# Kernel optimization log

Hardware: AMD Instinct MI355X
Metric: run time of the kernel (lower is better)

The kernel has to match this reference:

```python
import jax, jax.numpy as jnp
import numpy as np

NUM_HEADS = 16
NEG_INF = -1000000.0  # matches torch masked_fill value


def setup_inputs() -> dict:
    key = jax.random.key(0)
    k1, k2, k3, k4, k5, k6 = jax.random.split(key, 6)
    N, S, E = 2, 2048, 1024
    x_encoder = jax.random.normal(k1, (N, S, E), dtype=jnp.float32)
    x_decoder = jax.random.normal(k2, (N, S, E), dtype=jnp.float32)
    mask = jax.random.randint(k3, (S, S), 0, 2, dtype=jnp.int32)
    W_qk = jax.random.normal(k4, (2 * E, E), dtype=jnp.float32) * (1.0 / np.sqrt(E))
    W_v = jax.random.normal(k5, (E, E), dtype=jnp.float32) * (1.0 / np.sqrt(E))
    W_o = jax.random.normal(k6, (E, E), dtype=jnp.float32) * (1.0 / np.sqrt(E))
    return {"x_encoder": x_encoder, "x_decoder": x_decoder, "mask": mask,
            "W_qk": W_qk, "W_v": W_v, "W_o": W_o}


def reference(x_encoder, x_decoder, mask, W_qk, W_v, W_o):
    N, S, E = x_encoder.shape
    H = NUM_HEADS
    hd = E // H
    # projections (no bias)
    qk = x_encoder @ W_qk.T            # (N, S, 2E)
    v = x_decoder @ W_v.T              # (N, S, E)
    qk = qk.reshape(N, S, H, 2 * hd).transpose(0, 2, 1, 3)  # (N, H, S, 2hd)
    v = v.reshape(N, S, H, hd).transpose(0, 2, 1, 3)         # (N, H, S, hd)
    q, k = qk[..., :hd], qk[..., hd:]
    # scaled dot-product attention with mask fill
    logits = jnp.einsum('bhqd,bhkd->bhqk', q, k) / jnp.sqrt(jnp.float32(hd))
    m = mask[None, None, :, :]  # expand_mask: 2D -> (1,1,S,S)
    logits = jnp.where(m == 0, jnp.float32(NEG_INF), logits)
    attn = jax.nn.softmax(logits, axis=-1)
    vals = jnp.einsum('bhqk,bhkd->bhqd', attn, v)            # (N, H, S, hd)
    vals = vals.transpose(0, 2, 1, 3).reshape(N, S, E)
    return vals @ W_o.T
```

## Files before the change

### kernel.cpp

```cpp
#include <hip/hip_runtime.h>

typedef __attribute__((ext_vector_type(8))) short short8;
typedef __attribute__((ext_vector_type(4))) float f32x4;
typedef __attribute__((ext_vector_type(4))) unsigned short u16x4;
typedef __attribute__((ext_vector_type(4))) unsigned int u32x4;

#define MFMA16(A,B,C) __builtin_amdgcn_mfma_f32_16x16x32_bf16(A,B,C,0,0,0)

__device__ __forceinline__ unsigned short f2bf(float f) {
  unsigned int u = __builtin_bit_cast(unsigned int, f);
  unsigned int r = (u + 0x7fffu + ((u >> 16) & 1u)) >> 16;
  return (unsigned short)r;
}

__device__ __forceinline__ unsigned int cvt_pk_bf16(float lo, float hi) {
  unsigned int r;
  asm("v_cvt_pk_bf16_f32 %0, %1, %2" : "=v"(r) : "v"(lo), "v"(hi));
  return r;
}

__device__ __forceinline__ f32x4 zero4() {
  f32x4 z; z.x = 0.f; z.y = 0.f; z.z = 0.f; z.w = 0.f; return z;
}

__device__ __forceinline__ void gl_lds16(const void* g, void* l) {
  __builtin_amdgcn_global_load_lds((const __attribute__((address_space(1))) void*)g,
                                   (__attribute__((address_space(3))) void*)l, 16, 0, 0);
}

__global__ __launch_bounds__(256) void cvt_all(const float* __restrict__ xe,
                                               const float* __restrict__ xd,
                                               const float* __restrict__ wqk,
                                               const float* __restrict__ wv,
                                               const float* __restrict__ wo,
                                               unsigned short* __restrict__ ws) {
  long i = (long)blockIdx.x * 256 + threadIdx.x;
  const float* src; unsigned short* dst; long o;
  if (i < 1048576)      { src = xe;  dst = ws;            o = i; }
  else if (i < 2097152) { src = xd;  dst = ws + 4194304;  o = i - 1048576; }
  else if (i < 2621440) { src = wqk; dst = ws + 8388608;  o = i - 2097152; }
  else if (i < 2883584) { src = wv;  dst = ws + 10485760; o = i - 2621440; }
  else                  { src = wo;  dst = ws + 11534336; o = i - 2883584; }
  float4 f = ((const float4*)src)[o];
  u16x4 r; r.x = f2bf(f.x); r.y = f2bf(f.y); r.z = f2bf(f.z); r.w = f2bf(f.w);
  ((u16x4*)dst)[o] = r;
}

__global__ __launch_bounds__(256) void mask_pack(const int* __restrict__ mask,
                                                 unsigned int* __restrict__ mbits) {
  int idx = blockIdx.x * 256 + threadIdx.x;
  int row = idx >> 6, wi = idx & 63;
  const int* p = mask + (long)row * 2048 + wi * 32;
  unsigned int bits = 0;
  #pragma unroll
  for (int j = 0; j < 32; j++) bits |= (p[j] != 0 ? 1u : 0u) << j;
  mbits[idx] = bits;
}

template <int MODE>
__global__ __launch_bounds__(256) void gemm_bt(const unsigned short* __restrict__ A,
                                               const unsigned short* __restrict__ B,
                                               void* __restrict__ Cv,
                                               int M, int N, int K) {
  __shared__ __align__(16) unsigned short As[128 * 64];
  __shared__ __align__(16) unsigned short Bs[128 * 64];
  const int tid = threadIdx.x;
  const int w = tid >> 6, l = tid & 63;
  const int wr = w >> 1, wc = w & 1;
  const long row0 = (long)blockIdx.y * 128;
  const long col0 = (long)blockIdx.x * 128;
  const int lr = l >> 3;
  const int lc = (l & 7) * 8;

  f32x4 acc[4][4];
  #pragma unroll
  for (int m = 0; m < 4; m++)
    #pragma unroll
    for (int n = 0; n < 4; n++) acc[m][n] = zero4();

  for (int k0 = 0; k0 < K; k0 += 64) {
    #pragma unroll
    for (int j = 0; j < 4; j++) {
      int slot = j * 4 + w;
      int row = slot * 8 + lr;
      gl_lds16(A + (row0 + row) * K + k0 + lc, &As[slot * 512]);
      gl_lds16(B + (col0 + row) * K + k0 + lc, &Bs[slot * 512]);
    }
    __syncthreads();
    #pragma unroll
    for (int kk = 0; kk < 2; kk++) {
      short8 a[4], b[4];
      #pragma unroll
      for (int m = 0; m < 4; m++)
        a[m] = *(const short8*)&As[(wr * 64 + m * 16 + (l & 15)) * 64 + kk * 32 + (l >> 4) * 8];
      #pragma unroll
      for (int n = 0; n < 4; n++)
        b[n] = *(const short8*)&Bs[(wc * 64 + n * 16 + (l & 15)) * 64 + kk * 32 + (l >> 4) * 8];
      #pragma unroll
      for (int m = 0; m < 4; m++)
        #pragma unroll
        for (int n = 0; n < 4; n++)
          acc[m][n] = MFMA16(a[m], b[n], acc[m][n]);
    }
    __syncthreads();
  }

  #pragma unroll
  for (int m = 0; m < 4; m++) {
    long rowb = row0 + wr * 64 + m * 16 + ((l >> 4) * 4);
    #pragma unroll
    for (int n = 0; n < 4; n++) {
      long colb = col0 + wc * 64 + n * 16 + (l & 15);
      if (MODE == 0) {
        unsigned short* C = (unsigned short*)Cv;
        #pragma unroll
        for (int r = 0; r < 4; r++) C[(rowb + r) * N + colb] = f2bf(acc[m][n][r]);
      } else if (MODE == 1) {
        unsigned short* C = (unsigned short*)Cv;
        long bb = rowb >> 11, s0 = rowb & 2047;
        u16x4 pk;
        pk.x = f2bf(acc[m][n][0]); pk.y = f2bf(acc[m][n][1]);
        pk.z = f2bf(acc[m][n][2]); pk.w = f2bf(acc[m][n][3]);
        *(u16x4*)&C[(bb * 1024 + colb) * 2048 + s0] = pk;
      } else {
        float* C = (float*)Cv;
        #pragma unroll
        for (int r = 0; r < 4; r++) C[(rowb + r) * N + colb] = acc[m][n][r];
      }
    }
  }
}

__global__ __launch_bounds__(256, 4) void attn(const unsigned short* __restrict__ qk,
                                               const unsigned short* __restrict__ vT,
                                               const unsigned int* __restrict__ mbits,
                                               unsigned short* __restrict__ vals) {
  __shared__ __align__(16) unsigned short Ks[2][64 * 64];
  __shared__ __align__(16) unsigned short Vs[2][64 * 64];
  const int tid = threadIdx.x;
  const int w = tid >> 6, l = tid & 63;
  const int b = blockIdx.z, h = blockIdx.y;
  const int q0 = blockIdx.x * 64;
  const int c = l & 15, g = l >> 4;
  const int lr = l >> 3, pg = l & 7;

  const int qrow = q0 + w * 16 + c;
  const unsigned short* qptr = qk + (long)(b * 2048 + qrow) * 2048 + h * 128;
  short8 bq0 = *(const short8*)&qptr[g * 8];
  short8 bq1 = *(const short8*)&qptr[32 + g * 8];

  const float SC = 0.125f * 1.4426950408889634f;
  const int sw0 = ((g)     ^ (c & 7)) * 8;
  const int sw1 = ((g + 4) ^ (c & 7)) * 8;
  const int sA = c + (((2 * g)     & 3) << 4);
  const int sB = c + (((2 * g + 1) & 3) << 4);
  const int gh = g >> 1;

  const unsigned int* mrowp = mbits + (long)qrow * 64;

  const unsigned short* kbase = qk + (long)b * 2048 * 2048 + h * 128 + 64;
  const unsigned short* vbase = vT + (long)((b * 16 + h) * 64) * 2048;
  const int srow = w * 8 + lr;
  const int sgg = pg ^ (lr & 7);

  float l_run = 0.f;
  f32x4 o[4];
  #pragma unroll
  for (int d = 0; d < 4; d++) o[d] = zero4();

  {
    #pragma unroll
    for (int j = 0; j < 2; j++) {
      int row = srow + j * 32;
      gl_lds16(kbase + (long)row * 2048 + sgg * 8, &Ks[0][(w + j * 4) * 512]);
      gl_lds16(vbase + (long)row * 2048 + sgg * 8, &Vs[0][(w + j * 4) * 512]);
    }
  }
  __syncthreads();

  for (int kv0 = 0; kv0 < 2048; kv0 += 64) {
    const int cur = (kv0 >> 6) & 1;

    if (kv0 + 64 < 2048) {
      #pragma unroll
      for (int j = 0; j < 2; j++) {
        int row = srow + j * 32;
        gl_lds16(kbase + (long)(kv0 + 64 + row) * 2048 + sgg * 8, &Ks[cur ^ 1][(w + j * 4) * 512]);
        gl_lds16(vbase + (long)row * 2048 + kv0 + 64 + sgg * 8, &Vs[cur ^ 1][(w + j * 4) * 512]);
      }
    }

    unsigned long long mw = *(const unsigned long long*)&mrowp[kv0 >> 5];

    f32x4 sf[4];
    #pragma unroll
    for (int kvq = 0; kvq < 4; kvq++) {
      int R = kvq * 16 + c;
      short8 ak0 = *(const short8*)&Ks[cur][R * 64 + sw0];
      short8 ak1 = *(const short8*)&Ks[cur][R * 64 + sw1];
      f32x4 z = zero4();
      z = MFMA16(ak0, bq0, z);
      z = MFMA16(ak1, bq1, z);
      sf[kvq] = z;
    }

    mw >>= (g * 4);
    unsigned int mlo = (unsigned int)mw, mhi = (unsigned int)(mw >> 32);
    float pv[16];
    float lsum = 0.f;
    #pragma unroll
    for (int kvq = 0; kvq < 4; kvq++) {
      unsigned int msel = (kvq < 2) ? mlo : mhi;
      #pragma unroll
      for (int r = 0; r < 4; r++) {
        float e = __builtin_amdgcn_exp2f(sf[kvq][r] * SC);
        unsigned int bit = (msel >> (((kvq & 1) << 4) + r)) & 1u;
        float p = bit ? e : 0.0f;
        pv[kvq * 4 + r] = p;
        lsum += p;
      }
    }
    l_run += lsum;

    unsigned int pk0[2], pk1[2], pk2[2], pk3[2];
    pk0[0] = cvt_pk_bf16(pv[0],  pv[1]);  pk0[1] = cvt_pk_bf16(pv[2],  pv[3]);
    pk1[0] = cvt_pk_bf16(pv[4],  pv[5]);  pk1[1] = cvt_pk_bf16(pv[6],  pv[7]);
    pk2[0] = cvt_pk_bf16(pv[8],  pv[9]);  pk2[1] = cvt_pk_bf16(pv[10], pv[11]);
    pk3[0] = cvt_pk_bf16(pv[12], pv[13]); pk3[1] = cvt_pk_bf16(pv[14], pv[15]);

    u32x4 a0, a1;
    {
      int t0, t1;
      t0 = __shfl((int)pk0[0], sA); t1 = __shfl((int)pk1[0], sA);
      a0.x = gh ? (unsigned)t1 : (unsigned)t0;
      t0 = __shfl((int)pk0[1], sA); t1 = __shfl((int)pk1[1], sA);
      a0.y = gh ? (unsigned)t1 : (unsigned)t0;
      t0 = __shfl((int)pk0[0], sB); t1 = __shfl((int)pk1[0], sB);
      a0.z = gh ? (unsigned)t1 : (unsigned)t0;
      t0 = __shfl((int)pk0[1], sB); t1 = __shfl((int)pk1[1], sB);
      a0.w = gh ? (unsigned)t1 : (unsigned)t0;
      t0 = __shfl((int)pk2[0], sA); t1 = __shfl((int)pk3[0], sA);
      a1.x = gh ? (unsigned)t1 : (unsigned)t0;
      t0 = __shfl((int)pk2[1], sA); t1 = __shfl((int)pk3[1], sA);
      a1.y = gh ? (unsigned)t1 : (unsigned)t0;
      t0 = __shfl((int)pk2[0], sB); t1 = __shfl((int)pk3[0], sB);
      a1.z = gh ? (unsigned)t1 : (unsigned)t0;
      t0 = __shfl((int)pk2[1], sB); t1 = __shfl((int)pk3[1], sB);
      a1.w = gh ? (unsigned)t1 : (unsigned)t0;
    }
    short8 pa0 = __builtin_bit_cast(short8, a0);
    short8 pa1 = __builtin_bit_cast(short8, a1);

    #pragma unroll
    for (int dt = 0; dt < 4; dt++) {
      int d = dt * 16 + c;
      short8 bv0 = *(const short8*)&Vs[cur][d * 64 + sw0];
      short8 bv1 = *(const short8*)&Vs[cur][d * 64 + sw1];
      o[dt] = MFMA16(pa0, bv0, o[dt]);
      o[dt] = MFMA16(pa1, bv1, o[dt]);
    }

    __syncthreads();
  }

  l_run += __shfl_xor(l_run, 16);
  l_run += __shfl_xor(l_run, 32);
  float linv = 1.0f / l_run;
  float l0 = __shfl(linv, g * 4 + 0);
  float l1 = __shfl(linv, g * 4 + 1);
  float l2 = __shfl(linv, g * 4 + 2);
  float l3 = __shfl(linv, g * 4 + 3);
  #pragma unroll
  for (int dt = 0; dt < 4; dt++) {
    long rowb = (long)b * 2048 + q0 + w * 16 + g * 4;
    int col = h * 64 + dt * 16 + c;
    vals[(rowb + 0) * 1024 + col] = f2bf(o[dt][0] * l0);
    vals[(rowb + 1) * 1024 + col] = f2bf(o[dt][1] * l1);
    vals[(rowb + 2) * 1024 + col] = f2bf(o[dt][2] * l2);
    vals[(rowb + 3) * 1024 + col] = f2bf(o[dt][3] * l3);
  }
}

extern "C" void kernel_launch(void* const* d_in, const int* in_sizes, int n_in,
                              void* d_out, int out_size, void* d_ws, size_t ws_size,
                              hipStream_t stream) {
  const float* xe  = (const float*)d_in[0];
  const float* xd  = (const float*)d_in[1];
  const int*   msk = (const int*)d_in[2];
  const float* wqk = (const float*)d_in[3];
  const float* wv  = (const float*)d_in[4];
  const float* wo  = (const float*)d_in[5];
  float* out = (float*)d_out;
  unsigned short* ws = (unsigned short*)d_ws;

  unsigned short* xe_bf  = ws;
  unsigned short* xd_bf  = ws + 4194304;
  unsigned short* wqk_bf = ws + 8388608;
  unsigned short* wv_bf  = ws + 10485760;
  unsigned short* wo_bf  = ws + 11534336;
  unsigned short* qkb    = ws + 12582912;
  unsigned short* vTb    = ws + 20971520;
  unsigned short* valb   = ws + 25165824;
  unsigned int*   mbits  = (unsigned int*)(ws + 29360128);

  cvt_all<<<12288, 256, 0, stream>>>(xe, xd, wqk, wv, wo, ws);
  mask_pack<<<512, 256, 0, stream>>>(msk, mbits);
  gemm_bt<0><<<dim3(16, 32), 256, 0, stream>>>(xe_bf, wqk_bf, qkb, 4096, 2048, 1024);
  gemm_bt<1><<<dim3(8, 32), 256, 0, stream>>>(xd_bf, wv_bf, vTb, 4096, 1024, 1024);
  attn<<<dim3(32, 16, 2), 256, 0, stream>>>(qkb, vTb, mbits, valb);
  gemm_bt<2><<<dim3(8, 32), 256, 0, stream>>>(valb, wo_bf, out, 4096, 1024, 1024);
}
```

Baseline: 167.3 us.

## Process two query tiles per wave and load V fragments directly from global

Each attention block now covers 128 query rows, with each wave handling two 16-row query tiles that share the same K tile in LDS. The V tile is no longer staged in shared memory. Each lane reads its V fragments straight from global memory into registers every iteration, which halves LDS usage and removes V LDS reads. The cost is more registers (occupancy hint lowered from 4 to 2), half as many blocks, and uncoalesced global V loads that are issued before the QK MFMAs and sit on the critical path.

```diff
diff --git a/kernel.cpp b/kernel.cpp
--- a/kernel.cpp
+++ b/kernel.cpp
@@ -131,23 +131,75 @@
   }
 }
 
-__global__ __launch_bounds__(256, 4) void attn(const unsigned short* __restrict__ qk,
+__device__ __forceinline__ void softmax_pack(const f32x4* sf, unsigned long long mw,
+                                             int g, int sA, int sB, int gh, float SC,
+                                             float& l_run, short8& pa0o, short8& pa1o) {
+  mw >>= (g * 4);
+  unsigned int mlo = (unsigned int)mw, mhi = (unsigned int)(mw >> 32);
+  float pv[16];
+  float lsum = 0.f;
+  #pragma unroll
+  for (int kvq = 0; kvq < 4; kvq++) {
+    unsigned int msel = (kvq < 2) ? mlo : mhi;
+    #pragma unroll
+    for (int r = 0; r < 4; r++) {
+      float e = __builtin_amdgcn_exp2f(sf[kvq][r] * SC);
+      unsigned int bit = (msel >> (((kvq & 1) << 4) + r)) & 1u;
+      float p = bit ? e : 0.0f;
+      pv[kvq * 4 + r] = p;
+      lsum += p;
+    }
+  }
+  l_run += lsum;
+
+  unsigned int pk0[2], pk1[2], pk2[2], pk3[2];
+  pk0[0] = cvt_pk_bf16(pv[0],  pv[1]);  pk0[1] = cvt_pk_bf16(pv[2],  pv[3]);
+  pk1[0] = cvt_pk_bf16(pv[4],  pv[5]);  pk1[1] = cvt_pk_bf16(pv[6],  pv[7]);
+  pk2[0] = cvt_pk_bf16(pv[8],  pv[9]);  pk2[1] = cvt_pk_bf16(pv[10], pv[11]);
+  pk3[0] = cvt_pk_bf16(pv[12], pv[13]); pk3[1] = cvt_pk_bf16(pv[14], pv[15]);
+
+  u32x4 a0, a1;
+  int t0, t1;
+  t0 = __shfl((int)pk0[0], sA); t1 = __shfl((int)pk1[0], sA);
+  a0.x = gh ? (unsigned)t1 : (unsigned)t0;
+  t0 = __shfl((int)pk0[1], sA); t1 = __shfl((int)pk1[1], sA);
+  a0.y = gh ? (unsigned)t1 : (unsigned)t0;
+  t0 = __shfl((int)pk0[0], sB); t1 = __shfl((int)pk1[0], sB);
+  a0.z = gh ? (unsigned)t1 : (unsigned)t0;
+  t0 = __shfl((int)pk0[1], sB); t1 = __shfl((int)pk1[1], sB);
+  a0.w = gh ? (unsigned)t1 : (unsigned)t0;
+  t0 = __shfl((int)pk2[0], sA); t1 = __shfl((int)pk3[0], sA);
+  a1.x = gh ? (unsigned)t1 : (unsigned)t0;
+  t0 = __shfl((int)pk2[1], sA); t1 = __shfl((int)pk3[1], sA);
+  a1.y = gh ? (unsigned)t1 : (unsigned)t0;
+  t0 = __shfl((int)pk2[0], sB); t1 = __shfl((int)pk3[0], sB);
+  a1.z = gh ? (unsigned)t1 : (unsigned)t0;
+  t0 = __shfl((int)pk2[1], sB); t1 = __shfl((int)pk3[1], sB);
+  a1.w = gh ? (unsigned)t1 : (unsigned)t0;
+  pa0o = __builtin_bit_cast(short8, a0);
+  pa1o = __builtin_bit_cast(short8, a1);
+}
+
+__global__ __launch_bounds__(256, 2) void attn(const unsigned short* __restrict__ qk,
                                                const unsigned short* __restrict__ vT,
                                                const unsigned int* __restrict__ mbits,
                                                unsigned short* __restrict__ vals) {
   __shared__ __align__(16) unsigned short Ks[2][64 * 64];
-  __shared__ __align__(16) unsigned short Vs[2][64 * 64];
   const int tid = threadIdx.x;
   const int w = tid >> 6, l = tid & 63;
   const int b = blockIdx.z, h = blockIdx.y;
-  const int q0 = blockIdx.x * 64;
+  const int q0 = blockIdx.x * 128;
   const int c = l & 15, g = l >> 4;
   const int lr = l >> 3, pg = l & 7;
 
-  const int qrow = q0 + w * 16 + c;
-  const unsigned short* qptr = qk + (long)(b * 2048 + qrow) * 2048 + h * 128;
-  short8 bq0 = *(const short8*)&qptr[g * 8];
-  short8 bq1 = *(const short8*)&qptr[32 + g * 8];
+  const int qa = q0 + w * 32 + c;
+  const int qb = qa + 16;
+  const unsigned short* qptrA = qk + (long)(b * 2048 + qa) * 2048 + h * 128;
+  const unsigned short* qptrB = qk + (long)(b * 2048 + qb) * 2048 + h * 128;
+  short8 bqA0 = *(const short8*)&qptrA[g * 8];
+  short8 bqA1 = *(const short8*)&qptrA[32 + g * 8];
+  short8 bqB0 = *(const short8*)&qptrB[g * 8];
+  short8 bqB1 = *(const short8*)&qptrB[32 + g * 8];
 
   const float SC = 0.125f * 1.4426950408889634f;
   const int sw0 = ((g)     ^ (c & 7)) * 8;
@@ -156,25 +208,23 @@
   const int sB = c + (((2 * g + 1) & 3) << 4);
   const int gh = g >> 1;
 
-  const unsigned int* mrowp = mbits + (long)qrow * 64;
+  const unsigned int* mrowA = mbits + (long)qa * 64;
+  const unsigned int* mrowB = mbits + (long)qb * 64;
 
   const unsigned short* kbase = qk + (long)b * 2048 * 2048 + h * 128 + 64;
   const unsigned short* vbase = vT + (long)((b * 16 + h) * 64) * 2048;
   const int srow = w * 8 + lr;
   const int sgg = pg ^ (lr & 7);
 
-  float l_run = 0.f;
-  f32x4 o[4];
-  #pragma unroll
-  for (int d = 0; d < 4; d++) o[d] = zero4();
-
-  {
-    #pragma unroll
-    for (int j = 0; j < 2; j++) {
-      int row = srow + j * 32;
-      gl_lds16(kbase + (long)row * 2048 + sgg * 8, &Ks[0][(w + j * 4) * 512]);
-      gl_lds16(vbase + (long)row * 2048 + sgg * 8, &Vs[0][(w + j * 4) * 512]);
-    }
+  float lA = 0.f, lB = 0.f;
+  f32x4 oA[4], oB[4];
+  #pragma unroll
+  for (int d = 0; d < 4; d++) { oA[d] = zero4(); oB[d] = zero4(); }
+
+  #pragma unroll
+  for (int j = 0; j < 2; j++) {
+    int row = srow + j * 32;
+    gl_lds16(kbase + (long)row * 2048 + sgg * 8, &Ks[0][(w + j * 4) * 512]);
   }
   __syncthreads();
 
@@ -185,99 +235,72 @@
       #pragma unroll
       for (int j = 0; j < 2; j++) {
         int row = srow + j * 32;
-        gl_lds16(kbase + (long)(kv0 + 64 + row) * 2048 + sgg * 8, &Ks[cur ^ 1][(w + j * 4) * 512]);
-        gl_lds16(vbase + (long)row * 2048 + kv0 + 64 + sgg * 8, &Vs[cur ^ 1][(w + j * 4) * 512]);
+        gl_lds16(kbase + (long)(kv0 + 64 + row) * 2048 + sgg * 8,
+                 &Ks[cur ^ 1][(w + j * 4) * 512]);
       }
     }
 
-    unsigned long long mw = *(const unsigned long long*)&mrowp[kv0 >> 5];
-
-    f32x4 sf[4];
+    short8 vf[8];
+    #pragma unroll
+    for (int dt = 0; dt < 4; dt++) {
+      const unsigned short* vp = vbase + (long)(dt * 16 + c) * 2048 + kv0;
+      vf[dt * 2]     = *(const short8*)&vp[g * 8];
+      vf[dt * 2 + 1] = *(const short8*)&vp[32 + g * 8];
+    }
+    unsigned long long mwA = *(const unsigned long long*)&mrowA[kv0 >> 5];
+    unsigned long long mwB = *(const unsigned long long*)&mrowB[kv0 >> 5];
+
+    f32x4 sfA[4], sfB[4];
     #pragma unroll
     for (int kvq = 0; kvq < 4; kvq++) {
       int R = kvq * 16 + c;
       short8 ak0 = *(const short8*)&Ks[cur][R * 64 + sw0];
       short8 ak1 = *(const short8*)&Ks[cur][R * 64 + sw1];
-      f32x4 z = zero4();
-      z = MFMA16(ak0, bq0, z);
-      z = MFMA16(ak1, bq1, z);
-      sf[kvq] = z;
-    }
-
-    mw >>= (g * 4);
-    unsigned int mlo = (unsigned int)mw, mhi = (unsigned int)(mw >> 32);
-    float pv[16];
-    float lsum = 0.f;
-    #pragma unroll
-    for (int kvq = 0; kvq < 4; kvq++) {
-      unsigned int msel = (kvq < 2) ? mlo : mhi;
-      #pragma unroll
-      for (int r = 0; r < 4; r++) {
-        float e = __builtin_amdgcn_exp2f(sf[kvq][r] * SC);
-        unsigned int bit = (msel >> (((kvq & 1) << 4) + r)) & 1u;
-        float p = bit ? e : 0.0f;
-        pv[kvq * 4 + r] = p;
-        lsum += p;
-      }
-    }
-    l_run += lsum;
-
-    unsigned int pk0[2], pk1[2], pk2[2], pk3[2];
-    pk0[0] = cvt_pk_bf16(pv[0],  pv[1]);  pk0[1] = cvt_pk_bf16(pv[2],  pv[3]);
-    pk1[0] = cvt_pk_bf16(pv[4],  pv[5]);  pk1[1] = cvt_pk_bf16(pv[6],  pv[7]);
-    pk2[0] = cvt_pk_bf16(pv[8],  pv[9]);  pk2[1] = cvt_pk_bf16(pv[10], pv[11]);
-    pk3[0] = cvt_pk_bf16(pv[12], pv[13]); pk3[1] = cvt_pk_bf16(pv[14], pv[15]);
-
-    u32x4 a0, a1;
-    {
-      int t0, t1;
-      t0 = __shfl((int)pk0[0], sA); t1 = __shfl((int)pk1[0], sA);
-      a0.x = gh ? (unsigned)t1 : (unsigned)t0;
-      t0 = __shfl((int)pk0[1], sA); t1 = __shfl((int)pk1[1], sA);
-      a0.y = gh ? (unsigned)t1 : (unsigned)t0;
-      t0 = __shfl((int)pk0[0], sB); t1 = __shfl((int)pk1[0], sB);
-      a0.z = gh ? (unsigned)t1 : (unsigned)t0;
-      t0 = __shfl((int)pk0[1], sB); t1 = __shfl((int)pk1[1], sB);
-      a0.w = gh ? (unsigned)t1 : (unsigned)t0;
-      t0 = __shfl((int)pk2[0], sA); t1 = __shfl((int)pk3[0], sA);
-      a1.x = gh ? (unsigned)t1 : (unsigned)t0;
-      t0 = __shfl((int)pk2[1], sA); t1 = __shfl((int)pk3[1], sA);
-      a1.y = gh ? (unsigned)t1 : (unsigned)t0;
-      t0 = __shfl((int)pk2[0], sB); t1 = __shfl((int)pk3[0], sB);
-      a1.z = gh ? (unsigned)t1 : (unsigned)t0;
-      t0 = __shfl((int)pk2[1], sB); t1 = __shfl((int)pk3[1], sB);
-      a1.w = gh ? (unsigned)t1 : (unsigned)t0;
-    }
-    short8 pa0 = __builtin_bit_cast(short8, a0);
-    short8 pa1 = __builtin_bit_cast(short8, a1);
+      f32x4 zA = zero4();
+      zA = MFMA16(ak0, bqA0, zA);
+      zA = MFMA16(ak1, bqA1, zA);
+      sfA[kvq] = zA;
+      f32x4 zB = zero4();
+      zB = MFMA16(ak0, bqB0, zB);
+      zB = MFMA16(ak1, bqB1, zB);
+      sfB[kvq] = zB;
+    }
+
+    short8 paA0, paA1, paB0, paB1;
+    softmax_pack(sfA, mwA, g, sA, sB, gh, SC, lA, paA0, paA1);
+    softmax_pack(sfB, mwB, g, sA, sB, gh, SC, lB, paB0, paB1);
 
     #pragma unroll
     for (int dt = 0; dt < 4; dt++) {
-      int d = dt * 16 + c;
-      short8 bv0 = *(const short8*)&Vs[cur][d * 64 + sw0];
-      short8 bv1 = *(const short8*)&Vs[cur][d * 64 + sw1];
-      o[dt] = MFMA16(pa0, bv0, o[dt]);
-      o[dt] = MFMA16(pa1, bv1, o[dt]);
+      oA[dt] = MFMA16(paA0, vf[dt * 2],     oA[dt]);
+      oA[dt] = MFMA16(paA1, vf[dt * 2 + 1], oA[dt]);
+      oB[dt] = MFMA16(paB0, vf[dt * 2],     oB[dt]);
+      oB[dt] = MFMA16(paB1, vf[dt * 2 + 1], oB[dt]);
     }
 
     __syncthreads();
   }
 
-  l_run += __shfl_xor(l_run, 16);
-  l_run += __shfl_xor(l_run, 32);
-  float linv = 1.0f / l_run;
-  float l0 = __shfl(linv, g * 4 + 0);
-  float l1 = __shfl(linv, g * 4 + 1);
-  float l2 = __shfl(linv, g * 4 + 2);
-  float l3 = __shfl(linv, g * 4 + 3);
+  lA += __shfl_xor(lA, 16); lA += __shfl_xor(lA, 32);
+  lB += __shfl_xor(lB, 16); lB += __shfl_xor(lB, 32);
+  float liA = 1.0f / lA, liB = 1.0f / lB;
+  float a0 = __shfl(liA, g * 4 + 0), a1 = __shfl(liA, g * 4 + 1);
+  float a2 = __shfl(liA, g * 4 + 2), a3 = __shfl(liA, g * 4 + 3);
+  float b0 = __shfl(liB, g * 4 + 0), b1 = __shfl(liB, g * 4 + 1);
+  float b2 = __shfl(liB, g * 4 + 2), b3 = __shfl(liB, g * 4 + 3);
   #pragma unroll
   for (int dt = 0; dt < 4; dt++) {
-    long rowb = (long)b * 2048 + q0 + w * 16 + g * 4;
+    long rowA = (long)b * 2048 + q0 + w * 32 + g * 4;
+    long rowB = rowA + 16;
     int col = h * 64 + dt * 16 + c;
-    vals[(rowb + 0) * 1024 + col] = f2bf(o[dt][0] * l0);
-    vals[(rowb + 1) * 1024 + col] = f2bf(o[dt][1] * l1);
-    vals[(rowb + 2) * 1024 + col] = f2bf(o[dt][2] * l2);
-    vals[(rowb + 3) * 1024 + col] = f2bf(o[dt][3] * l3);
+    vals[(rowA + 0) * 1024 + col] = f2bf(oA[dt][0] * a0);
+    vals[(rowA + 1) * 1024 + col] = f2bf(oA[dt][1] * a1);
+    vals[(rowA + 2) * 1024 + col] = f2bf(oA[dt][2] * a2);
+    vals[(rowA + 3) * 1024 + col] = f2bf(oA[dt][3] * a3);
+    vals[(rowB + 0) * 1024 + col] = f2bf(oB[dt][0] * b0);
+    vals[(rowB + 1) * 1024 + col] = f2bf(oB[dt][1] * b1);
+    vals[(rowB + 2) * 1024 + col] = f2bf(oB[dt][2] * b2);
+    vals[(rowB + 3) * 1024 + col] = f2bf(oB[dt][3] * b3);
   }
 }
 
@@ -307,6 +330,6 @@
   mask_pack<<<512, 256, 0, stream>>>(msk, mbits);
   gemm_bt<0><<<dim3(16, 32), 256, 0, stream>>>(xe_bf, wqk_bf, qkb, 4096, 2048, 1024);
   gemm_bt<1><<<dim3(8, 32), 256, 0, stream>>>(xd_bf, wv_bf, vTb, 4096, 1024, 1024);
-  attn<<<dim3(32, 16, 2), 256, 0, stream>>>(qkb, vTb, mbits, valb);
+  attn<<<dim3(16, 16, 2), 256, 0, stream>>>(qkb, vTb, mbits, valb);
   gemm_bt<2><<<dim3(8, 32), 256, 0, stream>>>(valb, wo_bf, out, 4096, 1024, 1024);
 }
```

Measured after the change: 210.3 us. 1.26x slower.
